# Kernel optimization log

Hardware: AMD Instinct MI355X
Metric: run time of the kernel (lower is better)

## Reference

```python
import jax, jax.numpy as jnp
import numpy as np

B, N, T, F_IN = 32, 512, 12, 128
K, CF, TF, PRED = 3, 64, 64, 12


def _cheb_polys(n, k):
    # identity adjacency -> scaled Laplacian = -I; T0=I, T1=-I, Tk = 2(-I)T_{k-1} - T_{k-2}
    L = -np.eye(n, dtype=np.float32)
    polys = [np.eye(n, dtype=np.float32)]
    if k > 1:
        polys.append(L.copy())
    for i in range(2, k):
        polys.append(2 * L @ polys[i - 1] - polys[i - 2])
    return jnp.asarray(np.stack(polys))  # (K, N, N)


def _conv2d(x, w, b, stride, pad):
    # x: (B,C,H,W), w: (O,I,kh,kw) torch layout
    y = jax.lax.conv_general_dilated(x, w, window_strides=stride, padding=pad,
                                     dimension_numbers=("NCHW", "OIHW", "NCHW"))
    return y + b[None, :, None, None]


def _block(x, cheb, theta, tw, tb, rw, rb, lg, lb, stride):
    # x: (B,N,Fin,T); cheb: (K,N,N); theta: (K,Fin,Fout)
    # fused Chebyshev conv over all t and k: out[b,m,o,t] = sum_{k,n,f} x[b,n,f,t] cheb[k,n,m] theta[k,f,o]
    s = jax.nn.relu(jnp.einsum("bnft,knm,kfo->bmot", x, cheb, theta))  # (B,N,CF,T)
    t = _conv2d(jnp.transpose(s, (0, 2, 1, 3)), tw, tb, (1, stride), ((0, 0), (1, 1)))  # (B,TF,N,T')
    r = _conv2d(jnp.transpose(x, (0, 2, 1, 3)), rw, rb, (1, stride), ((0, 0), (0, 0)))  # (B,TF,N,T')
    h = jnp.transpose(jax.nn.relu(r + t), (0, 3, 2, 1))  # (B,T',N,TF)
    mu = h.mean(-1, keepdims=True)
    var = ((h - mu) ** 2).mean(-1, keepdims=True)
    h = (h - mu) * jax.lax.rsqrt(var + 1e-5) * lg + lb
    return jnp.transpose(h, (0, 2, 3, 1))  # (B,N,TF,T')


def setup_inputs() -> dict:
    key = jax.random.key(0)
    ks = jax.random.split(key, 8)
    rn = lambda k, shape, s=0.05: jax.random.normal(k, shape, dtype=jnp.float32) * s
    return {
        "x": jax.random.normal(ks[0], (B, N, T, F_IN), dtype=jnp.float32),
        "theta0": rn(ks[1], (K, F_IN, CF)),
        "tconv_w0": rn(ks[2], (TF, CF, 1, 3)),
        "tconv_b0": jnp.zeros((TF,), jnp.float32),
        "rconv_w0": rn(ks[3], (TF, F_IN, 1, 1)),
        "rconv_b0": jnp.zeros((TF,), jnp.float32),
        "ln_g0": jnp.ones((TF,), jnp.float32),
        "ln_b0": jnp.zeros((TF,), jnp.float32),
        "theta1": rn(ks[4], (K, TF, CF)),
        "tconv_w1": rn(ks[5], (TF, CF, 1, 3)),
        "tconv_b1": jnp.zeros((TF,), jnp.float32),
        "rconv_w1": rn(ks[6], (TF, TF, 1, 1)),
        "rconv_b1": jnp.zeros((TF,), jnp.float32),
        "ln_g1": jnp.ones((TF,), jnp.float32),
        "ln_b1": jnp.zeros((TF,), jnp.float32),
        "fconv_w": rn(ks[7], (PRED, T, 1, TF)),
        "fconv_b": jnp.zeros((PRED,), jnp.float32),
    }


def reference(x, theta0, tconv_w0, tconv_b0, rconv_w0, rconv_b0, ln_g0, ln_b0,
              theta1, tconv_w1, tconv_b1, rconv_w1, rconv_b1, ln_g1, ln_b1,
              fconv_w, fconv_b):
    cheb = _cheb_polys(x.shape[1], theta0.shape[0])
    h = jnp.transpose(x, (0, 1, 3, 2))  # (B,N,F_in,T)
    h = _block(h, cheb, theta0, tconv_w0, tconv_b0, rconv_w0, rconv_b0, ln_g0, ln_b0, 1)
    h = _block(h, cheb, theta1, tconv_w1, tconv_b1, rconv_w1, rconv_b1, ln_g1, ln_b1, 1)
    hf = jnp.transpose(h, (0, 3, 1, 2))  # (B,T',N,TF)
    out = _conv2d(hf, fconv_w, fconv_b, (1, 1), ((0, 0), (0, 0)))[:, :, :, -1]  # (B,PRED,N)
    return jnp.transpose(out, (0, 2, 1))  # (B,N,PRED)
```

## Files before the change

### kernel.cpp

```cpp
#include <hip/hip_runtime.h>
#include <hip/hip_bf16.h>


typedef __attribute__((ext_vector_type(8))) short bf16x8;
typedef __attribute__((ext_vector_type(4))) float f32x4;

#define FR_W1   0
#define FR_TW0  32
#define FR_W2   56
#define FR_TW1  72
#define FR_FW   96
#define N_FRAGS 120

__device__ __forceinline__ unsigned short f2bf(float f) {
    unsigned u = __builtin_bit_cast(unsigned, f);
    return (unsigned short)((u + 0x7FFFu + ((u >> 16) & 1u)) >> 16);
}

__device__ __forceinline__ unsigned short hcvt(float f) {
    union { __hip_bfloat16 h; unsigned short u; } cv;
    cv.h = __float2bfloat16(f);
    return cv.u;
}

__global__ void prep(const float* __restrict__ th0, const float* __restrict__ tw0,
                     const float* __restrict__ rw0, const float* __restrict__ th1,
                     const float* __restrict__ tw1, const float* __restrict__ rw1,
                     const float* __restrict__ fw,  short* __restrict__ wsb)
{
    int e = blockIdx.x * 256 + threadIdx.x;
    if (e >= N_FRAGS * 512) return;
    int frag = e >> 9;
    int l    = (e >> 3) & 63;
    int i    = e & 7;
    int kif  = ((l >> 4) << 3) + i;
    int nif  = l & 15;
    float val = 0.f;
    if (frag < 32) {
        int ks = frag >> 3, nt = frag & 7;
        int k = ks * 32 + kif, n = nt * 16 + nif;
        if (n < 64) val = th0[k*64+n] - th0[8192 + k*64+n] + th0[16384 + k*64+n];
        else        val = rw0[(n - 64) * 128 + k];
    } else if (frag < 56) {
        int q = frag - 32; int dt = q >> 3, ks = (q >> 2) & 1, nt = q & 3;
        int c = ks * 32 + kif, o = nt * 16 + nif;
        val = tw0[o * 192 + c * 3 + dt];
    } else if (frag < 72) {
        int q = frag - 56; int ks = q >> 3, nt = q & 7;
        int k = ks * 32 + kif, n = nt * 16 + nif;
        if (n < 64) val = th1[k*64+n] - th1[4096 + k*64+n] + th1[8192 + k*64+n];
        else        val = rw1[(n - 64) * 64 + k];
    } else if (frag < 96) {
        int q = frag - 72; int dt = q >> 3, ks = (q >> 2) & 1, nt = q & 3;
        int c = ks * 32 + kif, o = nt * 16 + nif;
        val = tw1[o * 192 + c * 3 + dt];
    } else {
        int ks = frag - 96; int k = ks * 32 + kif; int po = nif;
        val = (po < 12) ? fw[po * 768 + k] : 0.f;
    }
    wsb[e] = (short)f2bf(val);
}

#define LDS_SY(w)  (LDS + (w) * 6144)
#define LDS_WB     (LDS + 24576)

__global__ __launch_bounds__(256, 2) void mstgcn_mfma(
    const float* __restrict__ x,   const short* __restrict__ wsb,
    const float* __restrict__ tb0, const float* __restrict__ rb0,
    const float* __restrict__ lg0, const float* __restrict__ lb0,
    const float* __restrict__ tb1, const float* __restrict__ rb1,
    const float* __restrict__ lg1, const float* __restrict__ lb1,
    const float* __restrict__ fb,  float* __restrict__ out)
{
    __shared__ __align__(16) char LDS[81920];

    const int lane = threadIdx.x & 63;
    const int wave = threadIdx.x >> 6;
    const int l15  = lane & 15;
    const int l4   = lane >> 4;
    const int pair0 = blockIdx.x * 16 + wave * 4;

    char* syB = LDS_SY(wave);
    char* WB  = LDS_WB;

    auto stage = [&](int f, int slot) {
        *(bf16x8*)(WB + slot * 1024 + lane * 16) =
            *(const bf16x8*)(wsb + f * 512 + lane * 8);
    };
    auto ldwb1 = [&](int f) -> bf16x8 {
        return *(const bf16x8*)(WB + f * 1024 + lane * 16);
    };
    auto ldwb2 = [&](int f) -> bf16x8 {
        return *(const bf16x8*)(WB + (f - 56) * 1024 + lane * 16);
    };
    auto ldfrag = [&](int f) -> bf16x8 {
        return *(const bf16x8*)(wsb + f * 512 + lane * 8);
    };

    int tA[3];
    long gbase[3];
    #pragma unroll
    for (int mt = 0; mt < 3; ++mt) {
        int r = mt * 16 + l15;
        int p = r / 12;
        tA[mt]   = r - p * 12;
        gbase[mt] = ((long)(pair0 + p) * 12 + tA[mt]) * 128;
    }

    #pragma unroll
    for (int q = 0; q < 14; ++q) {
        int f = wave * 14 + q;
        stage(f, f);
    }

    bf16x8 aC[12];
    #pragma unroll
    for (int ks = 0; ks < 4; ++ks)
        #pragma unroll
        for (int mt = 0; mt < 3; ++mt) {
            const float* p = x + gbase[mt] + ks * 32 + l4 * 8;
            float v[8];
            *(float4*)(v)     = *(const float4*)(p);
            *(float4*)(v + 4) = *(const float4*)(p + 4);
            bf16x8 af;
            #pragma unroll
            for (int j = 0; j < 8; ++j) af[j] = (short)hcvt(v[j]);
            aC[ks * 3 + mt] = af;
        }
    __syncthreads();

    f32x4 accS[3][4] = {}, accR[3][4] = {};
    #pragma unroll
    for (int ks = 0; ks < 4; ++ks) {
        #pragma unroll
        for (int nt = 0; nt < 4; ++nt) {
            bf16x8 b = ldwb1(FR_W1 + ks * 8 + nt);
            #pragma unroll
            for (int mt = 0; mt < 3; ++mt)
                accS[mt][nt] = __builtin_amdgcn_mfma_f32_16x16x32_bf16(aC[ks * 3 + mt], b, accS[mt][nt], 0, 0, 0);
        }
        #pragma unroll
        for (int nt = 0; nt < 4; ++nt) {
            bf16x8 b = ldwb1(FR_W1 + ks * 8 + 4 + nt);
            #pragma unroll
            for (int mt = 0; mt < 3; ++mt)
                accR[mt][nt] = __builtin_amdgcn_mfma_f32_16x16x32_bf16(aC[ks * 3 + mt], b, accR[mt][nt], 0, 0, 0);
        }
    }
    #pragma unroll
    for (int mt = 0; mt < 3; ++mt)
        #pragma unroll
        for (int j = 0; j < 4; ++j) {
            int row = mt * 16 + l4 * 4 + j;
            int sw  = (row & 7) << 4;
            #pragma unroll
            for (int nt = 0; nt < 4; ++nt) {
                int col = nt * 16 + l15;
                *(short*)(syB + row * 128 + ((col * 2) ^ sw)) =
                    (short)hcvt(fmaxf(accS[mt][nt][j], 0.f));
            }
        }

    #pragma unroll
    for (int dt = 0; dt < 3; ++dt) {
        #pragma unroll
        for (int ks = 0; ks < 2; ++ks) {
            bf16x8 a[3];
            #pragma unroll
            for (int mt = 0; mt < 3; ++mt) {
                int ts    = tA[mt] + dt - 1;
                bool ok   = (ts >= 0) && (ts < 12);
                int srow  = ok ? (mt * 16 + l15 + dt - 1) : (mt * 16 + l15);
                int kb    = (ks * 32 + l4 * 8) * 2;
                bf16x8 av = *(const bf16x8*)(syB + srow * 128 + (kb ^ ((srow & 7) << 4)));
                a[mt] = ok ? av : (bf16x8)(short)0;
            }
            #pragma unroll
            for (int nt = 0; nt < 4; ++nt) {
                bf16x8 b = ldwb1(FR_TW0 + dt * 8 + ks * 4 + nt);
                #pragma unroll
                for (int mt = 0; mt < 3; ++mt)
                    accR[mt][nt] = __builtin_amdgcn_mfma_f32_16x16x32_bf16(a[mt], b, accR[mt][nt], 0, 0, 0);
            }
        }
    }
    __syncthreads();

    #pragma unroll
    for (int q = 0; q < 10; ++q) {
        int f = 56 + wave * 10 + q;
        stage(f, f - 56);
    }

    {
        float bv[4], lgv[4], lbv[4];
        #pragma unroll
        for (int nt = 0; nt < 4; ++nt) {
            int col = nt * 16 + l15;
            bv[nt]  = rb0[col] + tb0[col];
            lgv[nt] = lg0[col];
            lbv[nt] = lb0[col];
        }
        #pragma unroll
        for (int mt = 0; mt < 3; ++mt)
            #pragma unroll
            for (int j = 0; j < 4; ++j) {
                float v[4], sm = 0.f, sq = 0.f;
                #pragma unroll
                for (int nt = 0; nt < 4; ++nt) {
                    v[nt] = fmaxf(accR[mt][nt][j] + bv[nt], 0.f);
                    sm += v[nt]; sq += v[nt] * v[nt];
                }
                #pragma unroll
                for (int m = 8; m; m >>= 1) {
                    sm += __shfl_xor(sm, m, 64);
                    sq += __shfl_xor(sq, m, 64);
                }
                float mu = sm * 0.015625f;
                float is = rsqrtf(sq * 0.015625f - mu * mu + 1e-5f);
                int row = mt * 16 + l4 * 4 + j;
                int sw  = (row & 7) << 4;
                #pragma unroll
                for (int nt = 0; nt < 4; ++nt) {
                    int col = nt * 16 + l15;
                    *(short*)(syB + row * 128 + ((col * 2) ^ sw)) =
                        (short)hcvt((v[nt] - mu) * is * lgv[nt] + lbv[nt]);
                }
            }
    }

    bf16x8 aC2[6];
    #pragma unroll
    for (int ks = 0; ks < 2; ++ks)
        #pragma unroll
        for (int mt = 0; mt < 3; ++mt) {
            int row = mt * 16 + l15;
            int kb  = (ks * 32 + l4 * 8) * 2;
            aC2[ks * 3 + mt] = *(const bf16x8*)(syB + row * 128 + (kb ^ ((row & 7) << 4)));
        }
    __syncthreads();

    #pragma unroll
    for (int mt = 0; mt < 3; ++mt)
        #pragma unroll
        for (int nt = 0; nt < 4; ++nt) { accS[mt][nt] = (f32x4)0.f; accR[mt][nt] = (f32x4)0.f; }
    #pragma unroll
    for (int ks = 0; ks < 2; ++ks) {
        #pragma unroll
        for (int nt = 0; nt < 4; ++nt) {
            bf16x8 b = ldwb2(FR_W2 + ks * 8 + nt);
            #pragma unroll
            for (int mt = 0; mt < 3; ++mt)
                accS[mt][nt] = __builtin_amdgcn_mfma_f32_16x16x32_bf16(aC2[ks * 3 + mt], b, accS[mt][nt], 0, 0, 0);
        }
        #pragma unroll
        for (int nt = 0; nt < 4; ++nt) {
            bf16x8 b = ldwb2(FR_W2 + ks * 8 + 4 + nt);
            #pragma unroll
            for (int mt = 0; mt < 3; ++mt)
                accR[mt][nt] = __builtin_amdgcn_mfma_f32_16x16x32_bf16(aC2[ks * 3 + mt], b, accR[mt][nt], 0, 0, 0);
        }
    }
    #pragma unroll
    for (int mt = 0; mt < 3; ++mt)
        #pragma unroll
        for (int j = 0; j < 4; ++j) {
            int row = mt * 16 + l4 * 4 + j;
            int sw  = (row & 7) << 4;
            #pragma unroll
            for (int nt = 0; nt < 4; ++nt) {
                int col = nt * 16 + l15;
                *(short*)(syB + row * 128 + ((col * 2) ^ sw)) =
                    (short)hcvt(fmaxf(accS[mt][nt][j], 0.f));
            }
        }

    #pragma unroll
    for (int dt = 0; dt < 3; ++dt) {
        #pragma unroll
        for (int ks = 0; ks < 2; ++ks) {
            bf16x8 a[3];
            #pragma unroll
            for (int mt = 0; mt < 3; ++mt) {
                int ts    = tA[mt] + dt - 1;
                bool ok   = (ts >= 0) && (ts < 12);
                int srow  = ok ? (mt * 16 + l15 + dt - 1) : (mt * 16 + l15);
                int kb    = (ks * 32 + l4 * 8) * 2;
                bf16x8 av = *(const bf16x8*)(syB + srow * 128 + (kb ^ ((srow & 7) << 4)));
                a[mt] = ok ? av : (bf16x8)(short)0;
            }
            #pragma unroll
            for (int nt = 0; nt < 4; ++nt) {
                bf16x8 b = ldwb2(FR_TW1 + dt * 8 + ks * 4 + nt);
                #pragma unroll
                for (int mt = 0; mt < 3; ++mt)
                    accR[mt][nt] = __builtin_amdgcn_mfma_f32_16x16x32_bf16(a[mt], b, accR[mt][nt], 0, 0, 0);
            }
        }
    }

    {
        float bv[4], lgv[4], lbv[4];
        #pragma unroll
        for (int nt = 0; nt < 4; ++nt) {
            int col = nt * 16 + l15;
            bv[nt]  = rb1[col] + tb1[col];
            lgv[nt] = lg1[col];
            lbv[nt] = lb1[col];
        }
        #pragma unroll
        for (int mt = 0; mt < 3; ++mt)
            #pragma unroll
            for (int j = 0; j < 4; ++j) {
                float v[4], sm = 0.f, sq = 0.f;
                #pragma unroll
                for (int nt = 0; nt < 4; ++nt) {
                    v[nt] = fmaxf(accR[mt][nt][j] + bv[nt], 0.f);
                    sm += v[nt]; sq += v[nt] * v[nt];
                }
                #pragma unroll
                for (int m = 8; m; m >>= 1) {
                    sm += __shfl_xor(sm, m, 64);
                    sq += __shfl_xor(sq, m, 64);
                }
                float mu = sm * 0.015625f;
                float is = rsqrtf(sq * 0.015625f - mu * mu + 1e-5f);
                int row = mt * 16 + l4 * 4 + j;
                int sw  = (row & 7) << 4;
                #pragma unroll
                for (int nt = 0; nt < 4; ++nt) {
                    int col = nt * 16 + l15;
                    *(short*)(syB + row * 128 + ((col * 2) ^ sw)) =
                        (short)hcvt((v[nt] - mu) * is * lgv[nt] + lbv[nt]);
                }
            }
    }

    {
        f32x4 acc0 = (f32x4)0.f, acc1 = (f32x4)0.f;
        int p   = (l15 < 4) ? l15 : 0;
        #pragma unroll
        for (int ks = 0; ks < 24; ks += 2) {
            {
                int t = ks >> 1, f0 = l4 * 8;
                int row = p * 12 + t;
                bf16x8 a = *(const bf16x8*)(syB + row * 128 + ((f0 * 2) ^ ((row & 7) << 4)));
                acc0 = __builtin_amdgcn_mfma_f32_16x16x32_bf16(a, ldfrag(FR_FW + ks), acc0, 0, 0, 0);
            }
            {
                int t = ks >> 1, f0 = 32 + l4 * 8;
                int row = p * 12 + t;
                bf16x8 a = *(const bf16x8*)(syB + row * 128 + ((f0 * 2) ^ ((row & 7) << 4)));
                acc1 = __builtin_amdgcn_mfma_f32_16x16x32_bf16(a, ldfrag(FR_FW + ks + 1), acc1, 0, 0, 0);
            }
        }
        if (l4 == 0 && l15 < 12) {
            float fbv = fb[l15];
            #pragma unroll
            for (int j = 0; j < 4; ++j)
                out[(long)(pair0 + j) * 12 + l15] = acc0[j] + acc1[j] + fbv;
        }
    }
}

extern "C" void kernel_launch(void* const* d_in, const int* in_sizes, int n_in,
                              void* d_out, int out_size, void* d_ws, size_t ws_size,
                              hipStream_t stream)
{
    (void)in_sizes; (void)n_in; (void)out_size; (void)ws_size;
    const float* x   = (const float*)d_in[0];
    const float* th0 = (const float*)d_in[1];
    const float* tw0 = (const float*)d_in[2];
    const float* tb0 = (const float*)d_in[3];
    const float* rw0 = (const float*)d_in[4];
    const float* rb0 = (const float*)d_in[5];
    const float* lg0 = (const float*)d_in[6];
    const float* lb0 = (const float*)d_in[7];
    const float* th1 = (const float*)d_in[8];
    const float* tw1 = (const float*)d_in[9];
    const float* tb1 = (const float*)d_in[10];
    const float* rw1 = (const float*)d_in[11];
    const float* rb1 = (const float*)d_in[12];
    const float* lg1 = (const float*)d_in[13];
    const float* lb1 = (const float*)d_in[14];
    const float* fw  = (const float*)d_in[15];
    const float* fb  = (const float*)d_in[16];
    float* out = (float*)d_out;
    short* wsb = (short*)d_ws;

    prep<<<240, 256, 0, stream>>>(th0, tw0, rw0, th1, tw1, rw1, fw, wsb);
    mstgcn_mfma<<<1024, 256, 0, stream>>>(x, wsb, tb0, rb0, lg0, lb0,
                                          tb1, rb1, lg1, lb1, fb, out);
}
```

Measured before the change: 52.90 us.

## Stage all weight fragments once via global_load_lds, use 6-wave blocks, DPP reductions

```diff
diff --git a/kernel.cpp b/kernel.cpp
--- a/kernel.cpp
+++ b/kernel.cpp
@@ -4,6 +4,9 @@
 
 typedef __attribute__((ext_vector_type(8))) short bf16x8;
 typedef __attribute__((ext_vector_type(4))) float f32x4;
+
+typedef __attribute__((address_space(1))) const unsigned int gu32;
+typedef __attribute__((address_space(3))) unsigned int lu32;
 
 #define FR_W1   0
 #define FR_TW0  32
@@ -21,6 +24,20 @@
     union { __hip_bfloat16 h; unsigned short u; } cv;
     cv.h = __float2bfloat16(f);
     return cv.u;
+}
+
+template <int CTRL>
+__device__ __forceinline__ float dpp_add(float v) {
+    int t = __builtin_amdgcn_update_dpp(0, __builtin_bit_cast(int, v),
+                                        CTRL, 0xf, 0xf, true);
+    return v + __builtin_bit_cast(float, t);
+}
+__device__ __forceinline__ float red16(float v) {
+    v = dpp_add<0xB1>(v);
+    v = dpp_add<0x4E>(v);
+    v = dpp_add<0x141>(v);
+    v = dpp_add<0x140>(v);
+    return v;
 }
 
 __global__ void prep(const float* __restrict__ th0, const float* __restrict__ tw0,
@@ -62,9 +79,9 @@
 }
 
 #define LDS_SY(w)  (LDS + (w) * 6144)
-#define LDS_WB     (LDS + 24576)
-
-__global__ __launch_bounds__(256, 2) void mstgcn_mfma(
+#define LDS_WB     (LDS + 36864)
+
+__global__ __launch_bounds__(384, 1) void mstgcn_mfma(
     const float* __restrict__ x,   const short* __restrict__ wsb,
     const float* __restrict__ tb0, const float* __restrict__ rb0,
     const float* __restrict__ lg0, const float* __restrict__ lb0,
@@ -72,76 +89,68 @@
     const float* __restrict__ lg1, const float* __restrict__ lb1,
     const float* __restrict__ fb,  float* __restrict__ out)
 {
-    __shared__ __align__(16) char LDS[81920];
+    __shared__ __align__(16) char LDS[159744];
 
     const int lane = threadIdx.x & 63;
     const int wave = threadIdx.x >> 6;
     const int l15  = lane & 15;
     const int l4   = lane >> 4;
-    const int pair0 = blockIdx.x * 16 + wave * 4;
+    const int pair0 = blockIdx.x * 24 + wave * 4;
+    const bool alive = (pair0 < 16384);
 
     char* syB = LDS_SY(wave);
     char* WB  = LDS_WB;
 
-    auto stage = [&](int f, int slot) {
-        *(bf16x8*)(WB + slot * 1024 + lane * 16) =
-            *(const bf16x8*)(wsb + f * 512 + lane * 8);
-    };
-    auto ldwb1 = [&](int f) -> bf16x8 {
+    auto ldwb = [&](int f) -> bf16x8 {
         return *(const bf16x8*)(WB + f * 1024 + lane * 16);
     };
-    auto ldwb2 = [&](int f) -> bf16x8 {
-        return *(const bf16x8*)(WB + (f - 56) * 1024 + lane * 16);
-    };
-    auto ldfrag = [&](int f) -> bf16x8 {
-        return *(const bf16x8*)(wsb + f * 512 + lane * 8);
-    };
+
+    #pragma unroll
+    for (int i = 0; i < 20; ++i) {
+        int f = wave * 20 + i;
+        __builtin_amdgcn_global_load_lds(
+            (gu32*)(wsb + f * 512 + lane * 8),
+            (lu32*)(WB + f * 1024), 16, 0, 0);
+    }
 
     int tA[3];
-    long gbase[3];
-    #pragma unroll
-    for (int mt = 0; mt < 3; ++mt) {
-        int r = mt * 16 + l15;
-        int p = r / 12;
-        tA[mt]   = r - p * 12;
-        gbase[mt] = ((long)(pair0 + p) * 12 + tA[mt]) * 128;
-    }
-
-    #pragma unroll
-    for (int q = 0; q < 14; ++q) {
-        int f = wave * 14 + q;
-        stage(f, f);
-    }
-
     bf16x8 aC[12];
-    #pragma unroll
-    for (int ks = 0; ks < 4; ++ks)
+    if (alive) {
         #pragma unroll
         for (int mt = 0; mt < 3; ++mt) {
-            const float* p = x + gbase[mt] + ks * 32 + l4 * 8;
-            float v[8];
-            *(float4*)(v)     = *(const float4*)(p);
-            *(float4*)(v + 4) = *(const float4*)(p + 4);
-            bf16x8 af;
-            #pragma unroll
-            for (int j = 0; j < 8; ++j) af[j] = (short)hcvt(v[j]);
-            aC[ks * 3 + mt] = af;
-        }
+            int r = mt * 16 + l15;
+            int p = r / 12;
+            tA[mt] = r - p * 12;
+            long gb = ((long)(pair0 + p) * 12 + tA[mt]) * 128;
+            #pragma unroll
+            for (int ks = 0; ks < 4; ++ks) {
+                const float* pp = x + gb + ks * 32 + l4 * 8;
+                float v[8];
+                *(float4*)(v)     = *(const float4*)(pp);
+                *(float4*)(v + 4) = *(const float4*)(pp + 4);
+                bf16x8 af;
+                #pragma unroll
+                for (int j = 0; j < 8; ++j) af[j] = (short)hcvt(v[j]);
+                aC[ks * 3 + mt] = af;
+            }
+        }
+    }
     __syncthreads();
+    if (!alive) return;
 
     f32x4 accS[3][4] = {}, accR[3][4] = {};
     #pragma unroll
     for (int ks = 0; ks < 4; ++ks) {
         #pragma unroll
         for (int nt = 0; nt < 4; ++nt) {
-            bf16x8 b = ldwb1(FR_W1 + ks * 8 + nt);
+            bf16x8 b = ldwb(FR_W1 + ks * 8 + nt);
             #pragma unroll
             for (int mt = 0; mt < 3; ++mt)
                 accS[mt][nt] = __builtin_amdgcn_mfma_f32_16x16x32_bf16(aC[ks * 3 + mt], b, accS[mt][nt], 0, 0, 0);
         }
         #pragma unroll
         for (int nt = 0; nt < 4; ++nt) {
-            bf16x8 b = ldwb1(FR_W1 + ks * 8 + 4 + nt);
+            bf16x8 b = ldwb(FR_W1 + ks * 8 + 4 + nt);
             #pragma unroll
             for (int mt = 0; mt < 3; ++mt)
                 accR[mt][nt] = __builtin_amdgcn_mfma_f32_16x16x32_bf16(aC[ks * 3 + mt], b, accR[mt][nt], 0, 0, 0);
@@ -177,19 +186,12 @@
             }
             #pragma unroll
             for (int nt = 0; nt < 4; ++nt) {
-                bf16x8 b = ldwb1(FR_TW0 + dt * 8 + ks * 4 + nt);
+                bf16x8 b = ldwb(FR_TW0 + dt * 8 + ks * 4 + nt);
                 #pragma unroll
                 for (int mt = 0; mt < 3; ++mt)
                     accR[mt][nt] = __builtin_amdgcn_mfma_f32_16x16x32_bf16(a[mt], b, accR[mt][nt], 0, 0, 0);
             }
         }
-    }
-    __syncthreads();
-
-    #pragma unroll
-    for (int q = 0; q < 10; ++q) {
-        int f = 56 + wave * 10 + q;
-        stage(f, f - 56);
     }
 
     {
@@ -211,11 +213,8 @@
                     v[nt] = fmaxf(accR[mt][nt][j] + bv[nt], 0.f);
                     sm += v[nt]; sq += v[nt] * v[nt];
                 }
-                #pragma unroll
-                for (int m = 8; m; m >>= 1) {
-                    sm += __shfl_xor(sm, m, 64);
-                    sq += __shfl_xor(sq, m, 64);
-                }
+                sm = red16(sm);
+                sq = red16(sq);
                 float mu = sm * 0.015625f;
                 float is = rsqrtf(sq * 0.015625f - mu * mu + 1e-5f);
                 int row = mt * 16 + l4 * 4 + j;
@@ -238,7 +237,6 @@
             int kb  = (ks * 32 + l4 * 8) * 2;
             aC2[ks * 3 + mt] = *(const bf16x8*)(syB + row * 128 + (kb ^ ((row & 7) << 4)));
         }
-    __syncthreads();
 
     #pragma unroll
     for (int mt = 0; mt < 3; ++mt)
@@ -248,14 +246,14 @@
     for (int ks = 0; ks < 2; ++ks) {
         #pragma unroll
         for (int nt = 0; nt < 4; ++nt) {
-            bf16x8 b = ldwb2(FR_W2 + ks * 8 + nt);
+            bf16x8 b = ldwb(FR_W2 + ks * 8 + nt);
             #pragma unroll
             for (int mt = 0; mt < 3; ++mt)
                 accS[mt][nt] = __builtin_amdgcn_mfma_f32_16x16x32_bf16(aC2[ks * 3 + mt], b, accS[mt][nt], 0, 0, 0);
         }
         #pragma unroll
         for (int nt = 0; nt < 4; ++nt) {
-            bf16x8 b = ldwb2(FR_W2 + ks * 8 + 4 + nt);
+            bf16x8 b = ldwb(FR_W2 + ks * 8 + 4 + nt);
             #pragma unroll
             for (int mt = 0; mt < 3; ++mt)
                 accR[mt][nt] = __builtin_amdgcn_mfma_f32_16x16x32_bf16(aC2[ks * 3 + mt], b, accR[mt][nt], 0, 0, 0);
@@ -291,7 +289,7 @@
             }
             #pragma unroll
             for (int nt = 0; nt < 4; ++nt) {
-                bf16x8 b = ldwb2(FR_TW1 + dt * 8 + ks * 4 + nt);
+                bf16x8 b = ldwb(FR_TW1 + dt * 8 + ks * 4 + nt);
                 #pragma unroll
                 for (int mt = 0; mt < 3; ++mt)
                     accR[mt][nt] = __builtin_amdgcn_mfma_f32_16x16x32_bf16(a[mt], b, accR[mt][nt], 0, 0, 0);
@@ -318,11 +316,8 @@
                     v[nt] = fmaxf(accR[mt][nt][j] + bv[nt], 0.f);
                     sm += v[nt]; sq += v[nt] * v[nt];
                 }
-                #pragma unroll
-                for (int m = 8; m; m >>= 1) {
-                    sm += __shfl_xor(sm, m, 64);
-                    sq += __shfl_xor(sq, m, 64);
-                }
+                sm = red16(sm);
+                sq = red16(sq);
                 float mu = sm * 0.015625f;
                 float is = rsqrtf(sq * 0.015625f - mu * mu + 1e-5f);
                 int row = mt * 16 + l4 * 4 + j;
@@ -345,13 +340,13 @@
                 int t = ks >> 1, f0 = l4 * 8;
                 int row = p * 12 + t;
                 bf16x8 a = *(const bf16x8*)(syB + row * 128 + ((f0 * 2) ^ ((row & 7) << 4)));
-                acc0 = __builtin_amdgcn_mfma_f32_16x16x32_bf16(a, ldfrag(FR_FW + ks), acc0, 0, 0, 0);
+                acc0 = __builtin_amdgcn_mfma_f32_16x16x32_bf16(a, ldwb(FR_FW + ks), acc0, 0, 0, 0);
             }
             {
                 int t = ks >> 1, f0 = 32 + l4 * 8;
                 int row = p * 12 + t;
                 bf16x8 a = *(const bf16x8*)(syB + row * 128 + ((f0 * 2) ^ ((row & 7) << 4)));
-                acc1 = __builtin_amdgcn_mfma_f32_16x16x32_bf16(a, ldfrag(FR_FW + ks + 1), acc1, 0, 0, 0);
+                acc1 = __builtin_amdgcn_mfma_f32_16x16x32_bf16(a, ldwb(FR_FW + ks + 1), acc1, 0, 0, 0);
             }
         }
         if (l4 == 0 && l15 < 12) {
@@ -389,6 +384,6 @@
     short* wsb = (short*)d_ws;
 
     prep<<<240, 256, 0, stream>>>(th0, tw0, rw0, th1, tw1, rw1, fw, wsb);
-    mstgcn_mfma<<<1024, 256, 0, stream>>>(x, wsb, tb0, rb0, lg0, lb0,
-                                          tb1, rb1, lg1, lb1, fb, out);
-}
+    mstgcn_mfma<<<683, 384, 0, stream>>>(x, wsb, tb0, rb0, lg0, lb0,
+                                         tb1, rb1, lg1, lb1, fb, out);
+}
```

After: 67.49 us. +27.6%, slower.
